# Optimization experiments

Measured on AMD Instinct MI355X. Metric: run time of the kernel, lower is better.

Reference implementation:

```python
import jax, jax.numpy as jnp
import numpy as np

B_, L_, DM, DI, N_, R_ = 8, 2048, 192, 384, 16, 12  # batch, seq, d_model, d_inner, d_state, dt_rank
LN_EPS = 1e-5


def setup_inputs() -> dict:
    key = jax.random.key(0)
    ks = jax.random.split(key, 7)
    x = jax.random.normal(ks[0], (B_, L_, DM), jnp.float32)
    W_in = (jax.random.normal(ks[1], (2 * DI, DM), jnp.float32) * 0.02)
    x_proj_w = (jax.random.normal(ks[2], (R_ + 2 * N_, DI), jnp.float32) * 0.02)
    dt_std = R_ ** (-0.5)
    dt_proj_w = jax.random.uniform(ks[3], (DI, R_), jnp.float32, -dt_std, dt_std)
    # dt bias init: inverse-softplus of dt ~ LogUniform(1e-3, 1e-1)
    dt = jnp.exp(jax.random.uniform(ks[4], (DI,), jnp.float32) * (np.log(0.1) - np.log(0.001)) + np.log(0.001))
    dt = jnp.clip(dt, 1e-4, None)
    dt_proj_b = dt + jnp.log(-jnp.expm1(-dt))
    # A_log init: log(1..N) repeated over d_inner
    A_logs = jnp.log(jnp.tile(jnp.arange(1, N_ + 1, dtype=jnp.float32), (DI, 1)))  # [DI, N]
    Ds = jnp.ones((DI,), jnp.float32)
    ln_gamma = jnp.ones((DI,), jnp.float32)
    ln_beta = jnp.zeros((DI,), jnp.float32)
    W_out = (jax.random.normal(ks[5], (DM, DI), jnp.float32) * 0.02)
    return dict(x=x, W_in=W_in, x_proj_w=x_proj_w, dt_proj_w=dt_proj_w,
                dt_proj_b=dt_proj_b, A_logs=A_logs, Ds=Ds,
                ln_gamma=ln_gamma, ln_beta=ln_beta, W_out=W_out)


def _selective_scan(u, delta, A, Bs, Cs, Ds):
    # u, delta: [B, L, DI]; A: [DI, N]; Bs, Cs: [B, L, N]; Ds: [DI]
    def step(h, inp):
        d_t, u_t, B_t, C_t = inp              # [B,DI], [B,DI], [B,N], [B,N]
        dA = jnp.exp(d_t[..., None] * A)       # [B,DI,N]
        h = dA * h + (d_t * u_t)[..., None] * B_t[:, None, :]
        y_t = jnp.einsum('bdn,bn->bd', h, C_t)
        return h, y_t

    h0 = jnp.zeros((u.shape[0], u.shape[2], A.shape[1]), u.dtype)
    seq = (jnp.moveaxis(delta, 1, 0), jnp.moveaxis(u, 1, 0),
           jnp.moveaxis(Bs, 1, 0), jnp.moveaxis(Cs, 1, 0))
    _, ys = jax.lax.scan(step, h0, seq)        # ys: [L,B,DI]
    return jnp.moveaxis(ys, 0, 1) + Ds * u     # [B,L,DI]


def reference(x, W_in, x_proj_w, dt_proj_w, dt_proj_b, A_logs, Ds, ln_gamma, ln_beta, W_out):
    # in_proj + SiLU, then split into (u, z)  (d_conv <= 1 branch, non-softmax version)
    xz = jax.nn.silu(x @ W_in.T)               # [B,L,2*DI]
    u, z = jnp.split(xz, 2, axis=-1)           # [B,L,DI] each
    # x -> (dt, B, C) projections (K = 1)
    dbl = jnp.einsum('bld,cd->blc', u, x_proj_w)          # [B,L,R+2N]
    dts = dbl[..., :R_] @ dt_proj_w.T                      # [B,L,DI]
    Bs = dbl[..., R_:R_ + N_]                              # [B,L,N]
    Cs = dbl[..., R_ + N_:]                                # [B,L,N]
    delta = jax.nn.softplus(dts + dt_proj_b)               # delta_bias + softplus
    A = -jnp.exp(A_logs)                                   # [DI,N]
    y = _selective_scan(u, delta, A, Bs, Cs, Ds)           # [B,L,DI]
    # out_norm (LayerNorm over d_inner)
    mu = jnp.mean(y, axis=-1, keepdims=True)
    var = jnp.var(y, axis=-1, keepdims=True)
    y = (y - mu) * jax.lax.rsqrt(var + LN_EPS) * ln_gamma + ln_beta
    # gate and out_proj
    y = y * z
    return y @ W_out.T                                     # [B,L,DM]
```

## Files before the change

kernel.cpp:

```cpp
#include <hip/hip_runtime.h>
#include <hip/hip_bf16.h>
#include <math.h>


#define ROWS 16384
#define NCHUNK 16
#define CLEN 128

typedef short bf16x8 __attribute__((ext_vector_type(8)));
typedef float f32x4 __attribute__((ext_vector_type(4)));

__device__ __forceinline__ unsigned short f2bf(float f) {
    unsigned u = __float_as_uint(f);
    return (unsigned short)((u + 0x7fffu + ((u >> 16) & 1u)) >> 16);
}
__device__ __forceinline__ float bf2f(unsigned short h) {
    return __uint_as_float(((unsigned)h) << 16);
}

template <int CTRL>
__device__ __forceinline__ float ror_add(float x) {
    int y = __builtin_amdgcn_update_dpp(0, __float_as_int(x), CTRL, 0xF, 0xF, true);
    return x + __int_as_float(y);
}
__device__ __forceinline__ float row16_sum(float p) {
    p = ror_add<0x128>(p);
    p = ror_add<0x124>(p);
    p = ror_add<0x122>(p);
    p = ror_add<0x121>(p);
    return p;
}

#define LDK 40
__global__ __launch_bounds__(256) void k1_gemm_silu(
    const float* __restrict__ x, const float* __restrict__ Win,
    float* __restrict__ u, float* __restrict__ z)
{
    __shared__ short Ah[128 * LDK];
    __shared__ short Al[128 * LDK];
    __shared__ short Bh[128 * LDK];
    __shared__ short Bl[128 * LDK];
    const int tid = threadIdx.x;
    const int lane = tid & 63;
    const int w = tid >> 6;
    const int wr = w >> 1, wc = w & 1;
    const int bm = blockIdx.x * 128;
    const int bn = blockIdx.y * 128;

    f32x4 acc[4][4];
#pragma unroll
    for (int i = 0; i < 4; ++i)
#pragma unroll
        for (int j = 0; j < 4; ++j) acc[i][j] = (f32x4)0.f;

    const int r16 = lane & 15, q4 = lane >> 4;

    for (int k0 = 0; k0 < 192; k0 += 32) {
#pragma unroll
        for (int i = 0; i < 4; ++i) {
            int p = tid + i * 256;
            int r = p >> 3, k4 = (p & 7) * 4;
            float4 av = *(const float4*)(x + (size_t)(bm + r) * 192 + k0 + k4);
            unsigned short hx = f2bf(av.x), hy = f2bf(av.y), hz = f2bf(av.z), hw = f2bf(av.w);
            unsigned hi0 = (unsigned)hx | ((unsigned)hy << 16);
            unsigned hi1 = (unsigned)hz | ((unsigned)hw << 16);
            unsigned short lx = f2bf(av.x - bf2f(hx)), ly = f2bf(av.y - bf2f(hy));
            unsigned short lz = f2bf(av.z - bf2f(hz)), lw = f2bf(av.w - bf2f(hw));
            unsigned lo0 = (unsigned)lx | ((unsigned)ly << 16);
            unsigned lo1 = (unsigned)lz | ((unsigned)lw << 16);
            int wi = r * (LDK / 2) + (k4 >> 1);
            ((unsigned*)Ah)[wi] = hi0; ((unsigned*)Ah)[wi + 1] = hi1;
            ((unsigned*)Al)[wi] = lo0; ((unsigned*)Al)[wi + 1] = lo1;

            float4 bv = *(const float4*)(Win + (size_t)(bn + r) * 192 + k0 + k4);
            hx = f2bf(bv.x); hy = f2bf(bv.y); hz = f2bf(bv.z); hw = f2bf(bv.w);
            hi0 = (unsigned)hx | ((unsigned)hy << 16);
            hi1 = (unsigned)hz | ((unsigned)hw << 16);
            lx = f2bf(bv.x - bf2f(hx)); ly = f2bf(bv.y - bf2f(hy));
            lz = f2bf(bv.z - bf2f(hz)); lw = f2bf(bv.w - bf2f(hw));
            lo0 = (unsigned)lx | ((unsigned)ly << 16);
            lo1 = (unsigned)lz | ((unsigned)lw << 16);
            ((unsigned*)Bh)[wi] = hi0; ((unsigned*)Bh)[wi + 1] = hi1;
            ((unsigned*)Bl)[wi] = lo0; ((unsigned*)Bl)[wi + 1] = lo1;
        }
        __syncthreads();

        bf16x8 ah[4], al[4];
#pragma unroll
        for (int mt = 0; mt < 4; ++mt) {
            int off = (wr * 64 + mt * 16 + r16) * LDK + q4 * 8;
            ah[mt] = *(const bf16x8*)(Ah + off);
            al[mt] = *(const bf16x8*)(Al + off);
        }
#pragma unroll
        for (int nt = 0; nt < 4; ++nt) {
            int off = (wc * 64 + nt * 16 + r16) * LDK + q4 * 8;
            bf16x8 bh = *(const bf16x8*)(Bh + off);
            bf16x8 bl = *(const bf16x8*)(Bl + off);
#pragma unroll
            for (int mt = 0; mt < 4; ++mt) {
                acc[mt][nt] = __builtin_amdgcn_mfma_f32_16x16x32_bf16(ah[mt], bh, acc[mt][nt], 0, 0, 0);
                acc[mt][nt] = __builtin_amdgcn_mfma_f32_16x16x32_bf16(ah[mt], bl, acc[mt][nt], 0, 0, 0);
                acc[mt][nt] = __builtin_amdgcn_mfma_f32_16x16x32_bf16(al[mt], bh, acc[mt][nt], 0, 0, 0);
            }
        }
        __syncthreads();
    }

    float* dst = (bn < 384) ? u : z;
    const int col0 = (bn < 384) ? bn : (bn - 384);
#pragma unroll
    for (int mt = 0; mt < 4; ++mt) {
#pragma unroll
        for (int nt = 0; nt < 4; ++nt) {
            int col = col0 + wc * 64 + nt * 16 + r16;
#pragma unroll
            for (int r = 0; r < 4; ++r) {
                int row = bm + wr * 64 + mt * 16 + q4 * 4 + r;
                float s = acc[mt][nt][r];
                dst[(size_t)row * 384 + col] = s / (1.f + __expf(-s));
            }
        }
    }
}

__global__ __launch_bounds__(256) void k2_proj(
    const float* __restrict__ u, const float* __restrict__ xpw,
    const float* __restrict__ dtw, const float* __restrict__ dtb,
    float* __restrict__ delta, float* __restrict__ Bso, float* __restrict__ Cso)
{
    __shared__ float As[64 * 68];
    __shared__ float Bs[64 * 53];
    __shared__ float dtwS[384 * 13];
    __shared__ float dblS[64 * 13];
    const int tid = threadIdx.x;
    const int tx = tid & 15, ty = tid >> 4;
    const int row0 = blockIdx.x * 64;

#pragma unroll
    for (int i = 0; i < 5; ++i) {
        int p = tid + i * 256;
        if (p < 1152) {
            int dd = p / 3, q = (p % 3) * 4;
            float4 v = *(const float4*)(dtw + dd * 12 + q);
            dtwS[dd * 13 + q + 0] = v.x;
            dtwS[dd * 13 + q + 1] = v.y;
            dtwS[dd * 13 + q + 2] = v.z;
            dtwS[dd * 13 + q + 3] = v.w;
        }
    }

    float acc[4][3];
#pragma unroll
    for (int i = 0; i < 4; ++i)
#pragma unroll
        for (int g = 0; g < 3; ++g) acc[i][g] = 0.f;

    for (int k0 = 0; k0 < 384; k0 += 64) {
#pragma unroll
        for (int i = 0; i < 4; ++i) {
            int p = tid + i * 256;
            int r = p >> 4, k4 = (p & 15) * 4;
            float4 v = *(const float4*)(u + (size_t)(row0 + r) * 384 + k0 + k4);
            As[(k4 + 0) * 68 + r] = v.x;
            As[(k4 + 1) * 68 + r] = v.y;
            As[(k4 + 2) * 68 + r] = v.z;
            As[(k4 + 3) * 68 + r] = v.w;
        }
#pragma unroll
        for (int i = 0; i < 3; ++i) {
            int p = tid + i * 256;
            int c = p >> 4, k4 = (p & 15) * 4;
            float4 v = make_float4(0.f, 0.f, 0.f, 0.f);
            if (c < 44) v = *(const float4*)(xpw + (size_t)c * 384 + k0 + k4);
            Bs[(k4 + 0) * 53 + c] = v.x;
            Bs[(k4 + 1) * 53 + c] = v.y;
            Bs[(k4 + 2) * 53 + c] = v.z;
            Bs[(k4 + 3) * 53 + c] = v.w;
        }
        __syncthreads();
#pragma unroll 8
        for (int kk = 0; kk < 64; ++kk) {
            float4 a = *(const float4*)(As + kk * 68 + ty * 4);
            float b0 = Bs[kk * 53 + tx];
            float b1 = Bs[kk * 53 + tx + 16];
            float b2 = Bs[kk * 53 + tx + 32];
            acc[0][0] = fmaf(a.x, b0, acc[0][0]);
            acc[1][0] = fmaf(a.y, b0, acc[1][0]);
            acc[2][0] = fmaf(a.z, b0, acc[2][0]);
            acc[3][0] = fmaf(a.w, b0, acc[3][0]);
            acc[0][1] = fmaf(a.x, b1, acc[0][1]);
            acc[1][1] = fmaf(a.y, b1, acc[1][1]);
            acc[2][1] = fmaf(a.z, b1, acc[2][1]);
            acc[3][1] = fmaf(a.w, b1, acc[3][1]);
            acc[0][2] = fmaf(a.x, b2, acc[0][2]);
            acc[1][2] = fmaf(a.y, b2, acc[1][2]);
            acc[2][2] = fmaf(a.z, b2, acc[2][2]);
            acc[3][2] = fmaf(a.w, b2, acc[3][2]);
        }
        __syncthreads();
    }

#pragma unroll
    for (int i = 0; i < 4; ++i) {
        int lr = ty * 4 + i;
        int row = row0 + lr;
#pragma unroll
        for (int g = 0; g < 3; ++g) {
            int c = g * 16 + tx;
            float s = acc[i][g];
            if (c < 12)      dblS[lr * 13 + c] = s;
            else if (c < 28) Bso[(size_t)row * 16 + (c - 12)] = s;
            else if (c < 44) Cso[(size_t)row * 16 + (c - 28)] = s;
        }
    }
    __syncthreads();

    for (int it = 0; it < 96; ++it) {
        int o = it * 256 + tid;
        int r = o / 384, d = o - r * 384;
        float s = dtb[d];
        const float* wr = dtwS + d * 13;
        const float* db = dblS + r * 13;
#pragma unroll
        for (int j = 0; j < 12; ++j) s = fmaf(db[j], wr[j], s);
        float sp = (s > 20.f) ? s : log1pf(__expf(s));
        delta[(size_t)(row0 + r) * 384 + d] = sp;
    }
}

__global__ __launch_bounds__(256) void k3a_scan1(
    const float* __restrict__ delta, const float* __restrict__ u,
    const float* __restrict__ Bsv, const float* __restrict__ A_logs,
    float* __restrict__ hf, float* __restrict__ Ssum)
{
    const int tid = threadIdx.x;
    const int n = tid & 15, dl = tid >> 4;
    const int c  = blockIdx.x & 15;
    const int dt = blockIdx.x >> 4;
    const int b  = blockIdx.y;
    const int d  = dt * 16 + dl;
    const int t0 = c * CLEN;

    const float Acoef = -__expf(A_logs[d * 16 + n]);
    const float* dp = delta + ((size_t)b * 2048 + t0) * 384 + d;
    const float* up = u     + ((size_t)b * 2048 + t0) * 384 + d;
    const float* Bp = Bsv   + ((size_t)b * 2048 + t0) * 16 + n;

    float pdt[8], put[8], pB[8];
#pragma unroll
    for (int i = 0; i < 8; ++i) {
        pdt[i] = dp[(size_t)i * 384]; put[i] = up[(size_t)i * 384]; pB[i] = Bp[i * 16];
    }

    float h = 0.f, S = 0.f;
    for (int g = 0; g < CLEN; g += 8) {
        float cdt[8], cut[8], cB[8];
#pragma unroll
        for (int i = 0; i < 8; ++i) { cdt[i] = pdt[i]; cut[i] = put[i]; cB[i] = pB[i]; }
        dp += 8 * 384; up += 8 * 384; Bp += 8 * 16;
        if (g + 8 < CLEN) {
#pragma unroll
            for (int i = 0; i < 8; ++i) {
                pdt[i] = dp[(size_t)i * 384]; put[i] = up[(size_t)i * 384]; pB[i] = Bp[i * 16];
            }
        }
        __builtin_amdgcn_sched_barrier(0);
#pragma unroll
        for (int i = 0; i < 8; ++i) {
            float dv = cdt[i];
            float a = __expf(dv * Acoef);
            h = fmaf(a, h, dv * cut[i] * cB[i]);
            S += dv;
        }
    }
    hf[(((size_t)b * 384 + d) * NCHUNK + c) * 16 + n] = h;
    if (n == 0) Ssum[((size_t)b * 384 + d) * NCHUNK + c] = S;
}

__global__ __launch_bounds__(256) void k3b_scan2(
    float* __restrict__ dy, const float* __restrict__ u,
    const float* __restrict__ Bsv, const float* __restrict__ Csv,
    const float* __restrict__ A_logs, const float* __restrict__ Ds,
    const float* __restrict__ hf, const float* __restrict__ Ssum)
{
    const int tid = threadIdx.x;
    const int n = tid & 15, dl = tid >> 4;
    const int c  = blockIdx.x & 15;
    const int dt = blockIdx.x >> 4;
    const int b  = blockIdx.y;
    const int d  = dt * 16 + dl;
    const int t0 = c * CLEN;

    const float Acoef = -__expf(A_logs[d * 16 + n]);
    const float Dd = Ds[d];

    float h = 0.f;
    {
        const float* hfp = hf + (((size_t)b * 384 + d) * NCHUNK) * 16 + n;
        const float* Sp  = Ssum + ((size_t)b * 384 + d) * NCHUNK;
        for (int j = 0; j < c; ++j) {
            float P = __expf(Acoef * Sp[j]);
            h = fmaf(P, h, hfp[j * 16]);
        }
    }

    float* yp       = dy  + ((size_t)b * 2048 + t0) * 384 + d;
    const float* up = u   + ((size_t)b * 2048 + t0) * 384 + d;
    const float* Bp = Bsv + ((size_t)b * 2048 + t0) * 16 + n;
    const float* Cp = Csv + ((size_t)b * 2048 + t0) * 16 + n;

    float pdt[8], put[8], pB[8], pC[8];
#pragma unroll
    for (int i = 0; i < 8; ++i) {
        pdt[i] = yp[(size_t)i * 384]; put[i] = up[(size_t)i * 384];
        pB[i] = Bp[i * 16];           pC[i] = Cp[i * 16];
    }
    const float* dp = yp + 8 * 384;
    float* yq = yp;

    for (int g = 0; g < CLEN; g += 8) {
        float cdt[8], cut[8], cB[8], cC[8];
#pragma unroll
        for (int i = 0; i < 8; ++i) { cdt[i] = pdt[i]; cut[i] = put[i]; cB[i] = pB[i]; cC[i] = pC[i]; }
        up += 8 * 384; Bp += 8 * 16; Cp += 8 * 16;
        if (g + 8 < CLEN) {
#pragma unroll
            for (int i = 0; i < 8; ++i) {
                pdt[i] = dp[(size_t)i * 384]; put[i] = up[(size_t)i * 384];
                pB[i] = Bp[i * 16];           pC[i] = Cp[i * 16];
            }
        }
        dp += 8 * 384;
        __builtin_amdgcn_sched_barrier(0);
#pragma unroll
        for (int i = 0; i < 8; ++i) {
            float dv = cdt[i];
            float a = __expf(dv * Acoef);
            h = fmaf(a, h, dv * cut[i] * cB[i]);
            float p = row16_sum(h * cC[i]);
            if (n == 0) yq[(size_t)i * 384] = fmaf(Dd, cut[i], p);
        }
        yq += 8 * 384;
    }
}

__global__ __launch_bounds__(256) void k4_ln_mul(
    float* __restrict__ y, const float* __restrict__ z,
    const float* __restrict__ gamma, const float* __restrict__ beta)
{
    const int tid = threadIdx.x;
    const int lane = tid & 63;
    const int w = tid >> 6;
    const size_t row = (size_t)blockIdx.x * 4 + w;
    float* yr = y + row * 384;
    const float* zr = z + row * 384;
    float v[6];
    float s1 = 0.f, s2 = 0.f;
#pragma unroll
    for (int j = 0; j < 6; ++j) {
        v[j] = yr[lane + j * 64];
        s1 += v[j];
        s2 = fmaf(v[j], v[j], s2);
    }
#pragma unroll
    for (int off = 32; off > 0; off >>= 1) {
        s1 += __shfl_xor(s1, off);
        s2 += __shfl_xor(s2, off);
    }
    float mu = s1 * (1.f / 384.f);
    float var = s2 * (1.f / 384.f) - mu * mu;
    float rs = rsqrtf(var + 1e-5f);
#pragma unroll
    for (int j = 0; j < 6; ++j) {
        int d = lane + j * 64;
        float o = (v[j] - mu) * rs * gamma[d] + beta[d];
        yr[d] = o * zr[d];
    }
}

__global__ __launch_bounds__(256) void k5_gemm_out(
    const float* __restrict__ yn, const float* __restrict__ Wout,
    float* __restrict__ out)
{
    __shared__ short Ah[128 * LDK];
    __shared__ short Al[128 * LDK];
    __shared__ short Bh[64 * LDK];
    __shared__ short Bl[64 * LDK];
    const int tid = threadIdx.x;
    const int lane = tid & 63;
    const int w = tid >> 6;
    const int wr = w >> 1, wc = w & 1;
    const int bm = blockIdx.x * 128;
    const int bn = blockIdx.y * 64;

    f32x4 acc[4][2];
#pragma unroll
    for (int i = 0; i < 4; ++i)
#pragma unroll
        for (int j = 0; j < 2; ++j) acc[i][j] = (f32x4)0.f;

    const int r16 = lane & 15, q4 = lane >> 4;

    for (int k0 = 0; k0 < 384; k0 += 32) {
#pragma unroll
        for (int i = 0; i < 4; ++i) {
            int p = tid + i * 256;
            int r = p >> 3, k4 = (p & 7) * 4;
            float4 av = *(const float4*)(yn + (size_t)(bm + r) * 384 + k0 + k4);
            unsigned short hx = f2bf(av.x), hy = f2bf(av.y), hz = f2bf(av.z), hw = f2bf(av.w);
            unsigned hi0 = (unsigned)hx | ((unsigned)hy << 16);
            unsigned hi1 = (unsigned)hz | ((unsigned)hw << 16);
            unsigned short lx = f2bf(av.x - bf2f(hx)), ly = f2bf(av.y - bf2f(hy));
            unsigned short lz = f2bf(av.z - bf2f(hz)), lw = f2bf(av.w - bf2f(hw));
            unsigned lo0 = (unsigned)lx | ((unsigned)ly << 16);
            unsigned lo1 = (unsigned)lz | ((unsigned)lw << 16);
            int wi = r * (LDK / 2) + (k4 >> 1);
            ((unsigned*)Ah)[wi] = hi0; ((unsigned*)Ah)[wi + 1] = hi1;
            ((unsigned*)Al)[wi] = lo0; ((unsigned*)Al)[wi + 1] = lo1;
        }
#pragma unroll
        for (int i = 0; i < 2; ++i) {
            int p = tid + i * 256;
            int r = p >> 3, k4 = (p & 7) * 4;
            float4 bv = *(const float4*)(Wout + (size_t)(bn + r) * 384 + k0 + k4);
            unsigned short hx = f2bf(bv.x), hy = f2bf(bv.y), hz = f2bf(bv.z), hw = f2bf(bv.w);
            unsigned hi0 = (unsigned)hx | ((unsigned)hy << 16);
            unsigned hi1 = (unsigned)hz | ((unsigned)hw << 16);
            unsigned short lx = f2bf(bv.x - bf2f(hx)), ly = f2bf(bv.y - bf2f(hy));
            unsigned short lz = f2bf(bv.z - bf2f(hz)), lw = f2bf(bv.w - bf2f(hw));
            unsigned lo0 = (unsigned)lx | ((unsigned)ly << 16);
            unsigned lo1 = (unsigned)lz | ((unsigned)lw << 16);
            int wi = r * (LDK / 2) + (k4 >> 1);
            ((unsigned*)Bh)[wi] = hi0; ((unsigned*)Bh)[wi + 1] = hi1;
            ((unsigned*)Bl)[wi] = lo0; ((unsigned*)Bl)[wi + 1] = lo1;
        }
        __syncthreads();

        bf16x8 ah[4], al[4];
#pragma unroll
        for (int mt = 0; mt < 4; ++mt) {
            int off = (wr * 64 + mt * 16 + r16) * LDK + q4 * 8;
            ah[mt] = *(const bf16x8*)(Ah + off);
            al[mt] = *(const bf16x8*)(Al + off);
        }
#pragma unroll
        for (int nt = 0; nt < 2; ++nt) {
            int off = (wc * 32 + nt * 16 + r16) * LDK + q4 * 8;
            bf16x8 bh = *(const bf16x8*)(Bh + off);
            bf16x8 bl = *(const bf16x8*)(Bl + off);
#pragma unroll
            for (int mt = 0; mt < 4; ++mt) {
                acc[mt][nt] = __builtin_amdgcn_mfma_f32_16x16x32_bf16(ah[mt], bh, acc[mt][nt], 0, 0, 0);
                acc[mt][nt] = __builtin_amdgcn_mfma_f32_16x16x32_bf16(ah[mt], bl, acc[mt][nt], 0, 0, 0);
                acc[mt][nt] = __builtin_amdgcn_mfma_f32_16x16x32_bf16(al[mt], bh, acc[mt][nt], 0, 0, 0);
            }
        }
        __syncthreads();
    }

#pragma unroll
    for (int mt = 0; mt < 4; ++mt) {
#pragma unroll
        for (int nt = 0; nt < 2; ++nt) {
            int col = bn + wc * 32 + nt * 16 + r16;
#pragma unroll
            for (int r = 0; r < 4; ++r) {
                int row = bm + wr * 64 + mt * 16 + q4 * 4 + r;
                out[(size_t)row * 192 + col] = acc[mt][nt][r];
            }
        }
    }
}

extern "C" void kernel_launch(void* const* d_in, const int* in_sizes, int n_in,
                              void* d_out, int out_size, void* d_ws, size_t ws_size,
                              hipStream_t stream) {
    const float* x    = (const float*)d_in[0];
    const float* Win  = (const float*)d_in[1];
    const float* xpw  = (const float*)d_in[2];
    const float* dtw  = (const float*)d_in[3];
    const float* dtb  = (const float*)d_in[4];
    const float* Alog = (const float*)d_in[5];
    const float* Dsv  = (const float*)d_in[6];
    const float* lng  = (const float*)d_in[7];
    const float* lnb  = (const float*)d_in[8];
    const float* Wout = (const float*)d_in[9];
    float* out = (float*)d_out;

    const size_t nU  = (size_t)ROWS * 384;
    const size_t nBC = (size_t)ROWS * 16;
    const size_t nHF = (size_t)8 * 384 * NCHUNK * 16;
    const size_t nS  = (size_t)8 * 384 * NCHUNK;
    const size_t need = (nU * 3 + nBC * 2 + nHF + nS) * sizeof(float);
    if (ws_size < need) return;

    float* u    = (float*)d_ws;
    float* z    = u + nU;
    float* dl   = z + nU;
    float* Bsv  = dl + nU;
    float* Csv  = Bsv + nBC;
    float* hf   = Csv + nBC;
    float* Ssum = hf + nHF;

    k1_gemm_silu<<<dim3(128, 6), 256, 0, stream>>>(x, Win, u, z);
    k2_proj<<<256, 256, 0, stream>>>(u, xpw, dtw, dtb, dl, Bsv, Csv);
    k3a_scan1<<<dim3(24 * NCHUNK, 8), 256, 0, stream>>>(dl, u, Bsv, Alog, hf, Ssum);
    k3b_scan2<<<dim3(24 * NCHUNK, 8), 256, 0, stream>>>(dl, u, Bsv, Csv, Alog, Dsv, hf, Ssum);
    k4_ln_mul<<<4096, 256, 0, stream>>>(dl, z, lng, lnb);
    k5_gemm_out<<<dim3(128, 3), 256, 0, stream>>>(dl, Wout, out);
}
```

Baseline: 318.5 us.

## Restructure chunked scan: per-thread 16-state registers, separate chunk-combine kernel

```diff
diff --git a/kernel.cpp b/kernel.cpp
--- a/kernel.cpp
+++ b/kernel.cpp
@@ -4,8 +4,8 @@
 
 
 #define ROWS 16384
-#define NCHUNK 16
-#define CLEN 128
+#define NCHUNK 64
+#define CLEN 32
 
 typedef short bf16x8 __attribute__((ext_vector_type(8)));
 typedef float f32x4 __attribute__((ext_vector_type(4)));
@@ -18,18 +18,7 @@
     return __uint_as_float(((unsigned)h) << 16);
 }
 
-template <int CTRL>
-__device__ __forceinline__ float ror_add(float x) {
-    int y = __builtin_amdgcn_update_dpp(0, __float_as_int(x), CTRL, 0xF, 0xF, true);
-    return x + __int_as_float(y);
-}
-__device__ __forceinline__ float row16_sum(float p) {
-    p = ror_add<0x128>(p);
-    p = ror_add<0x124>(p);
-    p = ror_add<0x122>(p);
-    p = ror_add<0x121>(p);
-    return p;
-}
+#define LOG2E 1.44269504088896f
 
 #define LDK 40
 __global__ __launch_bounds__(256) void k1_gemm_silu(
@@ -229,119 +218,181 @@
     }
 }
 
-__global__ __launch_bounds__(256) void k3a_scan1(
+__global__ __launch_bounds__(384) void k3a_scan1(
     const float* __restrict__ delta, const float* __restrict__ u,
     const float* __restrict__ Bsv, const float* __restrict__ A_logs,
     float* __restrict__ hf, float* __restrict__ Ssum)
 {
     const int tid = threadIdx.x;
-    const int n = tid & 15, dl = tid >> 4;
-    const int c  = blockIdx.x & 15;
-    const int dt = blockIdx.x >> 4;
-    const int b  = blockIdx.y;
-    const int d  = dt * 16 + dl;
+    const int lane = tid & 63;
+    const int wv = tid >> 6;
+    const int c = blockIdx.x;
+    const int b = blockIdx.y;
+    const int d = wv * 64 + lane;
     const int t0 = c * CLEN;
 
-    const float Acoef = -__expf(A_logs[d * 16 + n]);
+    float Ac[16];
+    {
+#pragma unroll
+        for (int q = 0; q < 4; ++q) {
+            float4 v = *(const float4*)(A_logs + d * 16 + q * 4);
+            Ac[q * 4 + 0] = -__expf(v.x) * LOG2E;
+            Ac[q * 4 + 1] = -__expf(v.y) * LOG2E;
+            Ac[q * 4 + 2] = -__expf(v.z) * LOG2E;
+            Ac[q * 4 + 3] = -__expf(v.w) * LOG2E;
+        }
+    }
+
     const float* dp = delta + ((size_t)b * 2048 + t0) * 384 + d;
     const float* up = u     + ((size_t)b * 2048 + t0) * 384 + d;
-    const float* Bp = Bsv   + ((size_t)b * 2048 + t0) * 16 + n;
-
-    float pdt[8], put[8], pB[8];
-#pragma unroll
-    for (int i = 0; i < 8; ++i) {
-        pdt[i] = dp[(size_t)i * 384]; put[i] = up[(size_t)i * 384]; pB[i] = Bp[i * 16];
-    }
-
-    float h = 0.f, S = 0.f;
-    for (int g = 0; g < CLEN; g += 8) {
-        float cdt[8], cut[8], cB[8];
-#pragma unroll
-        for (int i = 0; i < 8; ++i) { cdt[i] = pdt[i]; cut[i] = put[i]; cB[i] = pB[i]; }
-        dp += 8 * 384; up += 8 * 384; Bp += 8 * 16;
-        if (g + 8 < CLEN) {
-#pragma unroll
-            for (int i = 0; i < 8; ++i) {
-                pdt[i] = dp[(size_t)i * 384]; put[i] = up[(size_t)i * 384]; pB[i] = Bp[i * 16];
-            }
+    const float* Bp = Bsv   + ((size_t)b * 2048 + t0) * 16;
+
+    float h[16];
+#pragma unroll
+    for (int n = 0; n < 16; ++n) h[n] = 0.f;
+    float S = 0.f;
+
+    float dv_n = dp[0], uv_n = up[0];
+    float4 B0n = *(const float4*)(Bp + 0);
+    float4 B1n = *(const float4*)(Bp + 4);
+    float4 B2n = *(const float4*)(Bp + 8);
+    float4 B3n = *(const float4*)(Bp + 12);
+
+    for (int s = 0; s < CLEN; ++s) {
+        float dv = dv_n, uv = uv_n;
+        float4 B0 = B0n, B1 = B1n, B2 = B2n, B3 = B3n;
+        if (s + 1 < CLEN) {
+            dp += 384; up += 384; Bp += 16;
+            dv_n = dp[0]; uv_n = up[0];
+            B0n = *(const float4*)(Bp + 0);
+            B1n = *(const float4*)(Bp + 4);
+            B2n = *(const float4*)(Bp + 8);
+            B3n = *(const float4*)(Bp + 12);
         }
         __builtin_amdgcn_sched_barrier(0);
-#pragma unroll
-        for (int i = 0; i < 8; ++i) {
-            float dv = cdt[i];
-            float a = __expf(dv * Acoef);
-            h = fmaf(a, h, dv * cut[i] * cB[i]);
-            S += dv;
-        }
-    }
-    hf[(((size_t)b * 384 + d) * NCHUNK + c) * 16 + n] = h;
-    if (n == 0) Ssum[((size_t)b * 384 + d) * NCHUNK + c] = S;
-}
-
-__global__ __launch_bounds__(256) void k3b_scan2(
+        S += dv;
+        float dvu = dv * uv;
+        float Br[16] = {B0.x, B0.y, B0.z, B0.w, B1.x, B1.y, B1.z, B1.w,
+                        B2.x, B2.y, B2.z, B2.w, B3.x, B3.y, B3.z, B3.w};
+#pragma unroll
+        for (int n = 0; n < 16; ++n) {
+            float a = exp2f(dv * Ac[n]);
+            h[n] = fmaf(a, h[n], dvu * Br[n]);
+        }
+    }
+
+    const size_t ho = (((size_t)b * NCHUNK + c) * 384 + d) * 16;
+#pragma unroll
+    for (int q = 0; q < 4; ++q)
+        *(float4*)(hf + ho + q * 4) = make_float4(h[q*4+0], h[q*4+1], h[q*4+2], h[q*4+3]);
+    Ssum[((size_t)b * NCHUNK + c) * 384 + d] = S;
+}
+
+__global__ __launch_bounds__(256) void k3c_combine(
+    float* __restrict__ hf, const float* __restrict__ Ssum,
+    const float* __restrict__ A_logs)
+{
+    const int tid = threadIdx.x;
+    const int n = tid & 15, dl = tid >> 4;
+    const int d = blockIdx.x * 16 + dl;
+    const int b = blockIdx.y;
+    const float Ac = -__expf(A_logs[d * 16 + n]) * LOG2E;
+
+    float h = 0.f;
+    for (int c = 0; c < NCHUNK; ++c) {
+        const size_t idx = (((size_t)b * NCHUNK + c) * 384 + d) * 16 + n;
+        float hfv = hf[idx];
+        float Sv  = Ssum[((size_t)b * NCHUNK + c) * 384 + d];
+        hf[idx] = h;
+        float P = exp2f(Ac * Sv);
+        h = fmaf(P, h, hfv);
+    }
+}
+
+__global__ __launch_bounds__(384) void k3b_scan2(
     float* __restrict__ dy, const float* __restrict__ u,
     const float* __restrict__ Bsv, const float* __restrict__ Csv,
     const float* __restrict__ A_logs, const float* __restrict__ Ds,
-    const float* __restrict__ hf, const float* __restrict__ Ssum)
-{
-    const int tid = threadIdx.x;
-    const int n = tid & 15, dl = tid >> 4;
-    const int c  = blockIdx.x & 15;
-    const int dt = blockIdx.x >> 4;
-    const int b  = blockIdx.y;
-    const int d  = dt * 16 + dl;
+    const float* __restrict__ hf)
+{
+    const int tid = threadIdx.x;
+    const int lane = tid & 63;
+    const int wv = tid >> 6;
+    const int c = blockIdx.x;
+    const int b = blockIdx.y;
+    const int d = wv * 64 + lane;
     const int t0 = c * CLEN;
 
-    const float Acoef = -__expf(A_logs[d * 16 + n]);
+    float Ac[16];
+#pragma unroll
+    for (int q = 0; q < 4; ++q) {
+        float4 v = *(const float4*)(A_logs + d * 16 + q * 4);
+        Ac[q * 4 + 0] = -__expf(v.x) * LOG2E;
+        Ac[q * 4 + 1] = -__expf(v.y) * LOG2E;
+        Ac[q * 4 + 2] = -__expf(v.z) * LOG2E;
+        Ac[q * 4 + 3] = -__expf(v.w) * LOG2E;
+    }
     const float Dd = Ds[d];
 
-    float h = 0.f;
+    float h[16];
     {
-        const float* hfp = hf + (((size_t)b * 384 + d) * NCHUNK) * 16 + n;
-        const float* Sp  = Ssum + ((size_t)b * 384 + d) * NCHUNK;
-        for (int j = 0; j < c; ++j) {
-            float P = __expf(Acoef * Sp[j]);
-            h = fmaf(P, h, hfp[j * 16]);
+        const size_t ho = (((size_t)b * NCHUNK + c) * 384 + d) * 16;
+#pragma unroll
+        for (int q = 0; q < 4; ++q) {
+            float4 v = *(const float4*)(hf + ho + q * 4);
+            h[q * 4 + 0] = v.x; h[q * 4 + 1] = v.y;
+            h[q * 4 + 2] = v.z; h[q * 4 + 3] = v.w;
         }
     }
 
     float* yp       = dy  + ((size_t)b * 2048 + t0) * 384 + d;
     const float* up = u   + ((size_t)b * 2048 + t0) * 384 + d;
-    const float* Bp = Bsv + ((size_t)b * 2048 + t0) * 16 + n;
-    const float* Cp = Csv + ((size_t)b * 2048 + t0) * 16 + n;
-
-    float pdt[8], put[8], pB[8], pC[8];
-#pragma unroll
-    for (int i = 0; i < 8; ++i) {
-        pdt[i] = yp[(size_t)i * 384]; put[i] = up[(size_t)i * 384];
-        pB[i] = Bp[i * 16];           pC[i] = Cp[i * 16];
-    }
-    const float* dp = yp + 8 * 384;
-    float* yq = yp;
-
-    for (int g = 0; g < CLEN; g += 8) {
-        float cdt[8], cut[8], cB[8], cC[8];
-#pragma unroll
-        for (int i = 0; i < 8; ++i) { cdt[i] = pdt[i]; cut[i] = put[i]; cB[i] = pB[i]; cC[i] = pC[i]; }
-        up += 8 * 384; Bp += 8 * 16; Cp += 8 * 16;
-        if (g + 8 < CLEN) {
-#pragma unroll
-            for (int i = 0; i < 8; ++i) {
-                pdt[i] = dp[(size_t)i * 384]; put[i] = up[(size_t)i * 384];
-                pB[i] = Bp[i * 16];           pC[i] = Cp[i * 16];
-            }
-        }
-        dp += 8 * 384;
+    const float* Bp = Bsv + ((size_t)b * 2048 + t0) * 16;
+    const float* Cp = Csv + ((size_t)b * 2048 + t0) * 16;
+
+    float dv_n = yp[0], uv_n = up[0];
+    float4 B0n = *(const float4*)(Bp + 0);
+    float4 B1n = *(const float4*)(Bp + 4);
+    float4 B2n = *(const float4*)(Bp + 8);
+    float4 B3n = *(const float4*)(Bp + 12);
+    float4 C0n = *(const float4*)(Cp + 0);
+    float4 C1n = *(const float4*)(Cp + 4);
+    float4 C2n = *(const float4*)(Cp + 8);
+    float4 C3n = *(const float4*)(Cp + 12);
+    const float* dpn = yp + 384;
+
+    for (int s = 0; s < CLEN; ++s) {
+        float dv = dv_n, uv = uv_n;
+        float4 B0 = B0n, B1 = B1n, B2 = B2n, B3 = B3n;
+        float4 C0 = C0n, C1 = C1n, C2 = C2n, C3 = C3n;
+        if (s + 1 < CLEN) {
+            up += 384; Bp += 16; Cp += 16;
+            dv_n = dpn[0]; uv_n = up[0];
+            B0n = *(const float4*)(Bp + 0);
+            B1n = *(const float4*)(Bp + 4);
+            B2n = *(const float4*)(Bp + 8);
+            B3n = *(const float4*)(Bp + 12);
+            C0n = *(const float4*)(Cp + 0);
+            C1n = *(const float4*)(Cp + 4);
+            C2n = *(const float4*)(Cp + 8);
+            C3n = *(const float4*)(Cp + 12);
+            dpn += 384;
+        }
         __builtin_amdgcn_sched_barrier(0);
-#pragma unroll
-        for (int i = 0; i < 8; ++i) {
-            float dv = cdt[i];
-            float a = __expf(dv * Acoef);
-            h = fmaf(a, h, dv * cut[i] * cB[i]);
-            float p = row16_sum(h * cC[i]);
-            if (n == 0) yq[(size_t)i * 384] = fmaf(Dd, cut[i], p);
-        }
-        yq += 8 * 384;
+        float dvu = dv * uv;
+        float Br[16] = {B0.x, B0.y, B0.z, B0.w, B1.x, B1.y, B1.z, B1.w,
+                        B2.x, B2.y, B2.z, B2.w, B3.x, B3.y, B3.z, B3.w};
+        float Cr[16] = {C0.x, C0.y, C0.z, C0.w, C1.x, C1.y, C1.z, C1.w,
+                        C2.x, C2.y, C2.z, C2.w, C3.x, C3.y, C3.z, C3.w};
+        float y = Dd * uv;
+#pragma unroll
+        for (int n = 0; n < 16; ++n) {
+            float a = exp2f(dv * Ac[n]);
+            h[n] = fmaf(a, h[n], dvu * Br[n]);
+            y = fmaf(Cr[n], h[n], y);
+        }
+        yp[0] = y;
+        yp += 384;
     }
 }
 
@@ -490,8 +541,8 @@
 
     const size_t nU  = (size_t)ROWS * 384;
     const size_t nBC = (size_t)ROWS * 16;
-    const size_t nHF = (size_t)8 * 384 * NCHUNK * 16;
-    const size_t nS  = (size_t)8 * 384 * NCHUNK;
+    const size_t nHF = (size_t)8 * NCHUNK * 384 * 16;
+    const size_t nS  = (size_t)8 * NCHUNK * 384;
     const size_t need = (nU * 3 + nBC * 2 + nHF + nS) * sizeof(float);
     if (ws_size < need) return;
 
@@ -505,8 +556,9 @@
 
     k1_gemm_silu<<<dim3(128, 6), 256, 0, stream>>>(x, Win, u, z);
     k2_proj<<<256, 256, 0, stream>>>(u, xpw, dtw, dtb, dl, Bsv, Csv);
-    k3a_scan1<<<dim3(24 * NCHUNK, 8), 256, 0, stream>>>(dl, u, Bsv, Alog, hf, Ssum);
-    k3b_scan2<<<dim3(24 * NCHUNK, 8), 256, 0, stream>>>(dl, u, Bsv, Csv, Alog, Dsv, hf, Ssum);
+    k3a_scan1<<<dim3(NCHUNK, 8), 384, 0, stream>>>(dl, u, Bsv, Alog, hf, Ssum);
+    k3c_combine<<<dim3(24, 8), 256, 0, stream>>>(hf, Ssum, Alog);
+    k3b_scan2<<<dim3(NCHUNK, 8), 384, 0, stream>>>(dl, u, Bsv, Csv, Alog, Dsv, hf);
     k4_ln_mul<<<4096, 256, 0, stream>>>(dl, z, lng, lnb);
     k5_gemm_out<<<dim3(128, 3), 256, 0, stream>>>(dl, Wout, out);
 }
```

New measurement: 300.9 us. -5.5%, faster.
